# Kernel optimization log

Measured on AMD Instinct MI355X. Metric: run time of the kernel, lower is better.

The kernel has to match this reference:

```python
import jax, jax.numpy as jnp
import numpy as np

EPS = 1e-5  # torch GroupNorm default eps

def setup_inputs() -> dict:
    key = jax.random.key(0)
    ks = jax.random.split(key, 6)
    B, H, W, C = 16, 64, 64, 768
    T, R = 8, 64
    x = jax.random.normal(ks[0], (B, H, W, C), dtype=jnp.float32)
    task_ids = jax.random.randint(ks[1], (B,), 0, T, dtype=jnp.int32)
    gamma = jnp.ones((C,), dtype=jnp.float32)
    beta = jnp.zeros((C,), dtype=jnp.float32)
    # kaiming-uniform-ish scale for down proj; up proj small (zeros in torch init,
    # but use small random so gradients are non-trivial)
    W_down = jax.random.normal(ks[2], (T, R, C), dtype=jnp.float32) / jnp.sqrt(jnp.float32(C))
    W_up = jax.random.normal(ks[3], (T, C, R), dtype=jnp.float32) * 0.02
    scales = jnp.ones((T,), dtype=jnp.float32)
    return {"x": x, "task_ids": task_ids, "gamma": gamma, "beta": beta,
            "W_down": W_down, "W_up": W_up, "scales": scales}

def reference(x, task_ids, gamma, beta, W_down, W_up, scales):
    # GroupNorm(num_groups=1): normalize each sample over (H, W, C), per-channel affine
    mean = jnp.mean(x, axis=(1, 2, 3), keepdims=True)
    var = jnp.var(x, axis=(1, 2, 3), keepdims=True)
    x_norm = (x - mean) * jax.lax.rsqrt(var + EPS) * gamma + beta  # [B,H,W,C]
    # Gather per-sample expert weights (1x1 convs == low-rank linear maps)
    Wd = W_down[task_ids]          # [B, R, C]
    Wu = W_up[task_ids]            # [B, C, R]
    s = scales[task_ids]           # [B]
    h = jnp.einsum('bhwc,brc->bhwr', x_norm, Wd)
    h = jax.nn.gelu(h, approximate=False)  # torch nn.GELU default is exact erf
    delta = jnp.einsum('bhwr,bcr->bhwc', h, Wu)
    return x + s[:, None, None, None] * delta
```

## Files before the change

### kernel.cpp

```cpp
#include <hip/hip_runtime.h>
#include <hip/hip_bf16.h>

#define BATCH 16
#define C 768
#define T 8
#define R 64
#define HW 4096
#define NPS (HW*C)
#define GN_EPS 1e-5f
#define NPART 48

typedef short bf16x8 __attribute__((ext_vector_type(8)));
typedef float f32x4 __attribute__((ext_vector_type(4)));

static __device__ __forceinline__ unsigned short f2bf(float f) {
    __hip_bfloat16 h = __float2bfloat16(f);
    return *reinterpret_cast<unsigned short*>(&h);
}

__global__ __launch_bounds__(256) void prep_stats_kernel(
        const float* __restrict__ Wdn, const float* __restrict__ Wup,
        const float* __restrict__ gamma, const float* __restrict__ beta,
        const float* __restrict__ x,
        float* __restrict__ partials,
        unsigned short* __restrict__ wdg, unsigned short* __restrict__ wu_bf,
        float* __restrict__ u, float* __restrict__ w) {
    int bid = blockIdx.x;
    int tid = threadIdx.x;
    if (bid < 768) {
        int idx = bid * 256 + tid;
        const int NF4 = T * R * C / 4;
        if (idx < NF4) {
            int c4 = idx % (C / 4);
            float4 v = ((const float4*)Wdn)[idx];
            float4 g = ((const float4*)gamma)[c4];
            ushort4 o;
            o.x = f2bf(v.x * g.x); o.y = f2bf(v.y * g.y);
            o.z = f2bf(v.z * g.z); o.w = f2bf(v.w * g.w);
            *reinterpret_cast<ushort4*>(wdg + idx * 4) = o;
        } else {
            int j = idx - NF4;
            float4 v = ((const float4*)Wup)[j];
            ushort4 o;
            o.x = f2bf(v.x); o.y = f2bf(v.y); o.z = f2bf(v.z); o.w = f2bf(v.w);
            *reinterpret_cast<ushort4*>(wu_bf + j * 4) = o;
        }
    } else if (bid < 896) {
        int rowid = (bid - 768) * 4 + (tid >> 6);
        int lane = tid & 63;
        const float* wrow = Wdn + (size_t)rowid * C;
        float su = 0.f, sw = 0.f;
        #pragma unroll
        for (int j = 0; j < 12; j++) {
            int c = lane + j * 64;
            float wv = wrow[c];
            su += wv * gamma[c];
            sw += wv * beta[c];
        }
        for (int off = 32; off > 0; off >>= 1) {
            su += __shfl_down(su, off);
            sw += __shfl_down(sw, off);
        }
        if (lane == 0) { u[rowid] = su; w[rowid] = sw; }
    } else {
        int sblk = bid - 896;
        int b = sblk / NPART, part = sblk % NPART;
        const float4* xp = (const float4*)(x + (size_t)b * NPS);
        float s = 0.f, q = 0.f;
        int base = part * 256 + tid;
        #pragma unroll 4
        for (int i = 0; i < 64; i++) {
            float4 v = xp[(size_t)i * 12288 + base];
            s += v.x + v.y + v.z + v.w;
            q += v.x*v.x + v.y*v.y + v.z*v.z + v.w*v.w;
        }
        for (int off = 32; off > 0; off >>= 1) {
            s += __shfl_down(s, off);
            q += __shfl_down(q, off);
        }
        __shared__ float ps[4], pq[4];
        int wave = tid >> 6, lane = tid & 63;
        if (lane == 0) { ps[wave] = s; pq[wave] = q; }
        __syncthreads();
        if (tid == 0) {
            float S = 0.f, Q = 0.f;
            #pragma unroll
            for (int wv = 0; wv < 4; wv++) { S += ps[wv]; Q += pq[wv]; }
            partials[(b * NPART + part) * 2]     = S;
            partials[(b * NPART + part) * 2 + 1] = Q;
        }
    }
}

__global__ __launch_bounds__(512, 1) void fused_kernel(
        const float* __restrict__ x, const int* __restrict__ task_ids,
        const float* __restrict__ scales, const float* __restrict__ partials,
        const unsigned short* __restrict__ wdg, const unsigned short* __restrict__ wu_bf,
        const float* __restrict__ u, const float* __restrict__ w,
        float* __restrict__ out) {
    __shared__ char xsb[3 * 49152];
    __shared__ char hsb[2][2048];

    int bid = blockIdx.x;
    int b = bid >> 4;
    int chunk = bid & 15;
    int tid = threadIdx.x;
    int wvid = tid >> 6, lane = tid & 63;
    int lr = lane & 15, lg = lane >> 4;
    int swz = (lr & 7) << 4;

    int t = task_ids[b];
    float sc = scales[t];

    float s1 = 0.f, s2 = 0.f;
    if (lane < NPART) {
        float2 v = ((const float2*)(partials + b * 2 * NPART))[lane];
        s1 = v.x; s2 = v.y;
    }
    #pragma unroll
    for (int off = 32; off > 0; off >>= 1) {
        s1 += __shfl_xor(s1, off);
        s2 += __shfl_xor(s2, off);
    }
    float mean = s1 * (1.f / NPS);
    float var  = s2 * (1.f / NPS) - mean * mean;
    float rstd = rsqrtf(var + GN_EPS);

    size_t base = (size_t)b * NPS + (size_t)chunk * 256 * C;
    const char* xbase_c = (const char*)(x + base);
    float* outp = out + base;

#define STAGE(ldbuf, tileidx) do {                                               \
    const char* _gs = xbase_c + (size_t)(tileidx) * 49152;                       \
    char* _ld = (ldbuf);                                                         \
    _Pragma("unroll")                                                            \
    for (int _jj = 0; _jj < 12; _jj++) {                                         \
        int _j = pw * 12 + _jj;                                                  \
        int _row = _j / 3;                                                       \
        int _sub = _j - _row * 3;                                                \
        int _cb = (_sub * 1024 + lane * 16) ^ ((_row & 7) << 4);                 \
        __builtin_amdgcn_global_load_lds(                                        \
            (const __attribute__((address_space(1))) void*)(_gs + _row * 3072 + _cb), \
            (__attribute__((address_space(3))) void*)(_ld + (size_t)_j * 1024),  \
            16, 0, 0);                                                           \
    }                                                                            \
} while (0)

    if (wvid < 4) {
        int pw = wvid;
        const unsigned short* wdp = wdg + t * (R * C);
        bf16x8 a1[24];
        #pragma unroll
        for (int k = 0; k < 24; k++)
            a1[k] = *reinterpret_cast<const bf16x8*>(wdp + (pw * 16 + lr) * C + k * 32 + lg * 8);

        int r0 = pw * 16 + lg * 4;
        float4 u4 = *reinterpret_cast<const float4*>(u + t * 64 + r0);
        float4 w4 = *reinterpret_cast<const float4*>(w + t * 64 + r0);
        float mb = rstd * mean;
        float bias0 = w4.x - mb * u4.x, bias1 = w4.y - mb * u4.y;
        float bias2 = w4.z - mb * u4.z, bias3 = w4.w - mb * u4.w;

        STAGE(xsb, 0);
        STAGE(xsb + 49152, 1);

        for (int i = 0; i < 16; i++) {
            if (i == 15) asm volatile("s_waitcnt vmcnt(0)" ::: "memory");
            else         asm volatile("s_waitcnt vmcnt(12)" ::: "memory");

            const char* xb = xsb + (i % 3) * 49152;
            f32x4 acc1a = {0.f, 0.f, 0.f, 0.f};
            f32x4 acc1b = {0.f, 0.f, 0.f, 0.f};
            #pragma unroll
            for (int k = 0; k < 24; k += 2) {
                #pragma unroll
                for (int kk = 0; kk < 2; kk++) {
                    int kc = k + kk;
                    int cb0 = (kc * 128 + lg * 32) ^ swz;
                    int cb1 = (kc * 128 + lg * 32 + 16) ^ swz;
                    f32x4 xv0 = *reinterpret_cast<const f32x4*>(xb + lr * 3072 + cb0);
                    f32x4 xv1 = *reinterpret_cast<const f32x4*>(xb + lr * 3072 + cb1);
                    bf16x8 bfrag;
                    bfrag[0] = (short)f2bf(xv0[0]); bfrag[1] = (short)f2bf(xv0[1]);
                    bfrag[2] = (short)f2bf(xv0[2]); bfrag[3] = (short)f2bf(xv0[3]);
                    bfrag[4] = (short)f2bf(xv1[0]); bfrag[5] = (short)f2bf(xv1[1]);
                    bfrag[6] = (short)f2bf(xv1[2]); bfrag[7] = (short)f2bf(xv1[3]);
                    if (kk == 0)
                        acc1a = __builtin_amdgcn_mfma_f32_16x16x32_bf16(a1[kc], bfrag, acc1a, 0, 0, 0);
                    else
                        acc1b = __builtin_amdgcn_mfma_f32_16x16x32_bf16(a1[kc], bfrag, acc1b, 0, 0, 0);
                }
            }
            float v0 = rstd * (acc1a[0] + acc1b[0]) + bias0;
            float v1 = rstd * (acc1a[1] + acc1b[1]) + bias1;
            float v2 = rstd * (acc1a[2] + acc1b[2]) + bias2;
            float v3 = rstd * (acc1a[3] + acc1b[3]) + bias3;
            ushort4 o;
            o.x = f2bf(0.5f * v0 * (1.f + erff(v0 * 0.70710678118f)));
            o.y = f2bf(0.5f * v1 * (1.f + erff(v1 * 0.70710678118f)));
            o.z = f2bf(0.5f * v2 * (1.f + erff(v2 * 0.70710678118f)));
            o.w = f2bf(0.5f * v3 * (1.f + erff(v3 * 0.70710678118f)));
            int hbyte = lr * 128 + ((pw * 32 + lg * 8) ^ swz);
            *reinterpret_cast<ushort4*>(hsb[i & 1] + hbyte) = o;

            asm volatile("s_waitcnt lgkmcnt(0)" ::: "memory");
            __builtin_amdgcn_s_barrier();
            if (i + 2 < 16) STAGE(xsb + ((i + 2) % 3) * 49152, i + 2);
        }
    } else {
        int cw = wvid - 4;
        const unsigned short* wup = wu_bf + t * (C * R);
        bf16x8 a2[12][2];
        #pragma unroll
        for (int cb = 0; cb < 12; cb++)
            #pragma unroll
            for (int ks = 0; ks < 2; ks++)
                a2[cb][ks] = *reinterpret_cast<const bf16x8*>(
                    wup + (cw * 192 + cb * 16 + lr) * R + ks * 32 + lg * 8);

        for (int i = 0; i < 16; i++) {
            if (i > 0) {
                int j = i - 1;
                const char* xb = xsb + (j % 3) * 49152;
                bf16x8 b2[2];
                #pragma unroll
                for (int ks = 0; ks < 2; ks++) {
                    int byte = lr * 128 + ((ks * 64 + lg * 16) ^ swz);
                    b2[ks] = *reinterpret_cast<const bf16x8*>(hsb[j & 1] + byte);
                }
                size_t ro = (size_t)(j * 16 + lr) * C;
                #pragma unroll
                for (int cb = 0; cb < 12; cb++) {
                    f32x4 acc = {0.f, 0.f, 0.f, 0.f};
                    acc = __builtin_amdgcn_mfma_f32_16x16x32_bf16(a2[cb][0], b2[0], acc, 0, 0, 0);
                    acc = __builtin_amdgcn_mfma_f32_16x16x32_bf16(a2[cb][1], b2[1], acc, 0, 0, 0);
                    int c0 = cw * 192 + cb * 16 + lg * 4;
                    float4 xr = *reinterpret_cast<const float4*>(xb + lr * 3072 + ((c0 * 4) ^ swz));
                    float4 ov;
                    ov.x = xr.x + sc * acc[0];
                    ov.y = xr.y + sc * acc[1];
                    ov.z = xr.z + sc * acc[2];
                    ov.w = xr.w + sc * acc[3];
                    *reinterpret_cast<float4*>(outp + ro + c0) = ov;
                }
            }
            __builtin_amdgcn_s_barrier();
        }
        {
            int j = 15;
            const char* xb = xsb + (j % 3) * 49152;
            bf16x8 b2[2];
            #pragma unroll
            for (int ks = 0; ks < 2; ks++) {
                int byte = lr * 128 + ((ks * 64 + lg * 16) ^ swz);
                b2[ks] = *reinterpret_cast<const bf16x8*>(hsb[j & 1] + byte);
            }
            size_t ro = (size_t)(j * 16 + lr) * C;
            #pragma unroll
            for (int cb = 0; cb < 12; cb++) {
                f32x4 acc = {0.f, 0.f, 0.f, 0.f};
                acc = __builtin_amdgcn_mfma_f32_16x16x32_bf16(a2[cb][0], b2[0], acc, 0, 0, 0);
                acc = __builtin_amdgcn_mfma_f32_16x16x32_bf16(a2[cb][1], b2[1], acc, 0, 0, 0);
                int c0 = cw * 192 + cb * 16 + lg * 4;
                float4 xr = *reinterpret_cast<const float4*>(xb + lr * 3072 + ((c0 * 4) ^ swz));
                float4 ov;
                ov.x = xr.x + sc * acc[0];
                ov.y = xr.y + sc * acc[1];
                ov.z = xr.z + sc * acc[2];
                ov.w = xr.w + sc * acc[3];
                *reinterpret_cast<float4*>(outp + ro + c0) = ov;
            }
        }
    }
#undef STAGE
}

extern "C" void kernel_launch(void* const* d_in, const int* in_sizes, int n_in,
                              void* d_out, int out_size, void* d_ws, size_t ws_size,
                              hipStream_t stream) {
    const float* x        = (const float*)d_in[0];
    const int*   task_ids = (const int*)d_in[1];
    const float* gamma    = (const float*)d_in[2];
    const float* beta     = (const float*)d_in[3];
    const float* W_down   = (const float*)d_in[4];
    const float* W_up     = (const float*)d_in[5];
    const float* scales   = (const float*)d_in[6];
    float* out = (float*)d_out;

    float* partials = (float*)d_ws;
    unsigned short* wdg   = (unsigned short*)((char*)d_ws + 8192);
    unsigned short* wu_bf = wdg + T * R * C;
    float* u = (float*)((char*)d_ws + 8192 + 2 * T * R * C * sizeof(unsigned short));
    float* w = u + T * R;

    prep_stats_kernel<<<1664, 256, 0, stream>>>(W_down, W_up, gamma, beta, x,
                                                partials, wdg, wu_bf, u, w);
    fused_kernel<<<256, 512, 0, stream>>>(x, task_ids, scales, partials,
                                          wdg, wu_bf, u, w, out);
}
```

Before: 116.8 us.

## Merge stats and weight prep into one cooperative kernel with grid sync

Folds the separate prep/statistics kernel into the main kernel, which now runs as a cooperative launch. Each block reduces its own chunk of x for the GroupNorm sums, publishes the partials, and waits on a grid-wide sync before using the per-sample statistics. Weight bf16 conversion, gamma folding and the u/w bias terms are computed per block from fp32 weights instead of in a prep pass. Output stores become nontemporal. This removes one kernel launch and the intermediate workspace round-trip, at the cost of redundant per-block weight conversion, a grid-wide barrier, and reading x twice within one kernel.

```diff
diff --git a/kernel.cpp b/kernel.cpp
--- a/kernel.cpp
+++ b/kernel.cpp
@@ -1,5 +1,6 @@
 #include <hip/hip_runtime.h>
 #include <hip/hip_bf16.h>
+#include <hip/hip_cooperative_groups.h>
 
 #define BATCH 16
 #define C 768
@@ -8,7 +9,6 @@
 #define HW 4096
 #define NPS (HW*C)
 #define GN_EPS 1e-5f
-#define NPART 48
 
 typedef short bf16x8 __attribute__((ext_vector_type(8)));
 typedef float f32x4 __attribute__((ext_vector_type(4)));
@@ -18,88 +18,16 @@
     return *reinterpret_cast<unsigned short*>(&h);
 }
 
-__global__ __launch_bounds__(256) void prep_stats_kernel(
+__global__ __launch_bounds__(512, 1) void fused_all(
+        const float* __restrict__ x, const int* __restrict__ task_ids,
+        const float* __restrict__ gamma, const float* __restrict__ beta,
         const float* __restrict__ Wdn, const float* __restrict__ Wup,
-        const float* __restrict__ gamma, const float* __restrict__ beta,
-        const float* __restrict__ x,
-        float* __restrict__ partials,
-        unsigned short* __restrict__ wdg, unsigned short* __restrict__ wu_bf,
-        float* __restrict__ u, float* __restrict__ w) {
-    int bid = blockIdx.x;
-    int tid = threadIdx.x;
-    if (bid < 768) {
-        int idx = bid * 256 + tid;
-        const int NF4 = T * R * C / 4;
-        if (idx < NF4) {
-            int c4 = idx % (C / 4);
-            float4 v = ((const float4*)Wdn)[idx];
-            float4 g = ((const float4*)gamma)[c4];
-            ushort4 o;
-            o.x = f2bf(v.x * g.x); o.y = f2bf(v.y * g.y);
-            o.z = f2bf(v.z * g.z); o.w = f2bf(v.w * g.w);
-            *reinterpret_cast<ushort4*>(wdg + idx * 4) = o;
-        } else {
-            int j = idx - NF4;
-            float4 v = ((const float4*)Wup)[j];
-            ushort4 o;
-            o.x = f2bf(v.x); o.y = f2bf(v.y); o.z = f2bf(v.z); o.w = f2bf(v.w);
-            *reinterpret_cast<ushort4*>(wu_bf + j * 4) = o;
-        }
-    } else if (bid < 896) {
-        int rowid = (bid - 768) * 4 + (tid >> 6);
-        int lane = tid & 63;
-        const float* wrow = Wdn + (size_t)rowid * C;
-        float su = 0.f, sw = 0.f;
-        #pragma unroll
-        for (int j = 0; j < 12; j++) {
-            int c = lane + j * 64;
-            float wv = wrow[c];
-            su += wv * gamma[c];
-            sw += wv * beta[c];
-        }
-        for (int off = 32; off > 0; off >>= 1) {
-            su += __shfl_down(su, off);
-            sw += __shfl_down(sw, off);
-        }
-        if (lane == 0) { u[rowid] = su; w[rowid] = sw; }
-    } else {
-        int sblk = bid - 896;
-        int b = sblk / NPART, part = sblk % NPART;
-        const float4* xp = (const float4*)(x + (size_t)b * NPS);
-        float s = 0.f, q = 0.f;
-        int base = part * 256 + tid;
-        #pragma unroll 4
-        for (int i = 0; i < 64; i++) {
-            float4 v = xp[(size_t)i * 12288 + base];
-            s += v.x + v.y + v.z + v.w;
-            q += v.x*v.x + v.y*v.y + v.z*v.z + v.w*v.w;
-        }
-        for (int off = 32; off > 0; off >>= 1) {
-            s += __shfl_down(s, off);
-            q += __shfl_down(q, off);
-        }
-        __shared__ float ps[4], pq[4];
-        int wave = tid >> 6, lane = tid & 63;
-        if (lane == 0) { ps[wave] = s; pq[wave] = q; }
-        __syncthreads();
-        if (tid == 0) {
-            float S = 0.f, Q = 0.f;
-            #pragma unroll
-            for (int wv = 0; wv < 4; wv++) { S += ps[wv]; Q += pq[wv]; }
-            partials[(b * NPART + part) * 2]     = S;
-            partials[(b * NPART + part) * 2 + 1] = Q;
-        }
-    }
-}
-
-__global__ __launch_bounds__(512, 1) void fused_kernel(
-        const float* __restrict__ x, const int* __restrict__ task_ids,
-        const float* __restrict__ scales, const float* __restrict__ partials,
-        const unsigned short* __restrict__ wdg, const unsigned short* __restrict__ wu_bf,
-        const float* __restrict__ u, const float* __restrict__ w,
-        float* __restrict__ out) {
+        const float* __restrict__ scales,
+        float* __restrict__ partials, float* __restrict__ out) {
     __shared__ char xsb[3 * 49152];
     __shared__ char hsb[2][2048];
+    __shared__ float uws[4][16][2];
+    __shared__ float red[8][2];
 
     int bid = blockIdx.x;
     int b = bid >> 4;
@@ -112,23 +40,25 @@
     int t = task_ids[b];
     float sc = scales[t];
 
-    float s1 = 0.f, s2 = 0.f;
-    if (lane < NPART) {
-        float2 v = ((const float2*)(partials + b * 2 * NPART))[lane];
-        s1 = v.x; s2 = v.y;
+    size_t basee = (size_t)b * NPS + (size_t)chunk * 256 * C;
+    const float4* xp4 = (const float4*)(x + basee);
+    const char* xbase_c = (const char*)(x + basee);
+    float* outp = out + basee;
+
+    {
+        float s = 0.f, q = 0.f;
+        #pragma unroll 16
+        for (int i = 0; i < 96; i++) {
+            float4 v = xp4[i * 512 + tid];
+            s += v.x + v.y + v.z + v.w;
+            q += v.x*v.x + v.y*v.y + v.z*v.z + v.w*v.w;
+        }
+        for (int off = 32; off > 0; off >>= 1) {
+            s += __shfl_down(s, off);
+            q += __shfl_down(q, off);
+        }
+        if (lane == 0) { red[wvid][0] = s; red[wvid][1] = q; }
     }
-    #pragma unroll
-    for (int off = 32; off > 0; off >>= 1) {
-        s1 += __shfl_xor(s1, off);
-        s2 += __shfl_xor(s2, off);
-    }
-    float mean = s1 * (1.f / NPS);
-    float var  = s2 * (1.f / NPS) - mean * mean;
-    float rstd = rsqrtf(var + GN_EPS);
-
-    size_t base = (size_t)b * NPS + (size_t)chunk * 256 * C;
-    const char* xbase_c = (const char*)(x + base);
-    float* outp = out + base;
 
 #define STAGE(ldbuf, tileidx) do {                                               \
     const char* _gs = xbase_c + (size_t)(tileidx) * 49152;                       \
@@ -148,18 +78,71 @@
 
     if (wvid < 4) {
         int pw = wvid;
-        const unsigned short* wdp = wdg + t * (R * C);
+
+        const float* wdp = Wdn + (size_t)t * R * C + (size_t)(pw * 16 + lr) * C;
         bf16x8 a1[24];
         #pragma unroll
-        for (int k = 0; k < 24; k++)
-            a1[k] = *reinterpret_cast<const bf16x8*>(wdp + (pw * 16 + lr) * C + k * 32 + lg * 8);
-
-        int r0 = pw * 16 + lg * 4;
-        float4 u4 = *reinterpret_cast<const float4*>(u + t * 64 + r0);
-        float4 w4 = *reinterpret_cast<const float4*>(w + t * 64 + r0);
+        for (int k = 0; k < 24; k++) {
+            int col = k * 32 + lg * 8;
+            float4 v0 = *reinterpret_cast<const float4*>(wdp + col);
+            float4 v1 = *reinterpret_cast<const float4*>(wdp + col + 4);
+            float4 g0 = *reinterpret_cast<const float4*>(gamma + col);
+            float4 g1 = *reinterpret_cast<const float4*>(gamma + col + 4);
+            bf16x8 a;
+            a[0] = (short)f2bf(v0.x * g0.x); a[1] = (short)f2bf(v0.y * g0.y);
+            a[2] = (short)f2bf(v0.z * g0.z); a[3] = (short)f2bf(v0.w * g0.w);
+            a[4] = (short)f2bf(v1.x * g1.x); a[5] = (short)f2bf(v1.y * g1.y);
+            a[6] = (short)f2bf(v1.z * g1.z); a[7] = (short)f2bf(v1.w * g1.w);
+            a1[k] = a;
+        }
+
+        {
+            const float* wrow = Wdn + ((size_t)t * R + (pw * 16 + lr)) * C + lg * 192;
+            const float4* wr4 = (const float4*)wrow;
+            const float4* g4  = (const float4*)(gamma + lg * 192);
+            const float4* b4  = (const float4*)(beta  + lg * 192);
+            float su = 0.f, sw = 0.f;
+            #pragma unroll 8
+            for (int j = 0; j < 48; j++) {
+                float4 wv = wr4[j], gv = g4[j], bv = b4[j];
+                su += wv.x*gv.x + wv.y*gv.y + wv.z*gv.z + wv.w*gv.w;
+                sw += wv.x*bv.x + wv.y*bv.y + wv.z*bv.z + wv.w*bv.w;
+            }
+            su += __shfl_xor(su, 16); su += __shfl_xor(su, 32);
+            sw += __shfl_xor(sw, 16); sw += __shfl_xor(sw, 32);
+            if (lg == 0) { uws[pw][lr][0] = su; uws[pw][lr][1] = sw; }
+        }
+
+        __syncthreads();
+        if (tid == 0) {
+            float S = 0.f, Q = 0.f;
+            #pragma unroll
+            for (int wv = 0; wv < 8; wv++) { S += red[wv][0]; Q += red[wv][1]; }
+            __hip_atomic_store(&partials[bid * 2],     S, __ATOMIC_RELEASE, __HIP_MEMORY_SCOPE_AGENT);
+            __hip_atomic_store(&partials[bid * 2 + 1], Q, __ATOMIC_RELEASE, __HIP_MEMORY_SCOPE_AGENT);
+        }
+        cooperative_groups::this_grid().sync();
+
+        float s1 = 0.f, s2 = 0.f;
+        if (lane < 16) {
+            s1 = __hip_atomic_load(&partials[(b * 16 + lane) * 2],     __ATOMIC_ACQUIRE, __HIP_MEMORY_SCOPE_AGENT);
+            s2 = __hip_atomic_load(&partials[(b * 16 + lane) * 2 + 1], __ATOMIC_ACQUIRE, __HIP_MEMORY_SCOPE_AGENT);
+        }
+        #pragma unroll
+        for (int off = 8; off > 0; off >>= 1) {
+            s1 += __shfl_xor(s1, off);
+            s2 += __shfl_xor(s2, off);
+        }
+        s1 = __shfl(s1, 0); s2 = __shfl(s2, 0);
+        float mean = s1 * (1.f / NPS);
+        float var  = s2 * (1.f / NPS) - mean * mean;
+        float rstd = rsqrtf(var + GN_EPS);
         float mb = rstd * mean;
-        float bias0 = w4.x - mb * u4.x, bias1 = w4.y - mb * u4.y;
-        float bias2 = w4.z - mb * u4.z, bias3 = w4.w - mb * u4.w;
+        int r00 = lg * 4;
+        float bias0 = uws[pw][r00+0][1] - mb * uws[pw][r00+0][0];
+        float bias1 = uws[pw][r00+1][1] - mb * uws[pw][r00+1][0];
+        float bias2 = uws[pw][r00+2][1] - mb * uws[pw][r00+2][0];
+        float bias3 = uws[pw][r00+3][1] - mb * uws[pw][r00+3][0];
 
         STAGE(xsb, 0);
         STAGE(xsb + 49152, 1);
@@ -167,6 +150,7 @@
         for (int i = 0; i < 16; i++) {
             if (i == 15) asm volatile("s_waitcnt vmcnt(0)" ::: "memory");
             else         asm volatile("s_waitcnt vmcnt(12)" ::: "memory");
+            __builtin_amdgcn_s_barrier();
 
             const char* xb = xsb + (i % 3) * 49152;
             f32x4 acc1a = {0.f, 0.f, 0.f, 0.f};
@@ -209,16 +193,30 @@
         }
     } else {
         int cw = wvid - 4;
-        const unsigned short* wup = wu_bf + t * (C * R);
+
+        const float* wup = Wup + (size_t)t * C * R;
         bf16x8 a2[12][2];
         #pragma unroll
-        for (int cb = 0; cb < 12; cb++)
-            #pragma unroll
-            for (int ks = 0; ks < 2; ks++)
-                a2[cb][ks] = *reinterpret_cast<const bf16x8*>(
-                    wup + (cw * 192 + cb * 16 + lr) * R + ks * 32 + lg * 8);
+        for (int cb = 0; cb < 12; cb++) {
+            #pragma unroll
+            for (int ks = 0; ks < 2; ks++) {
+                const float* src = wup + (size_t)(cw * 192 + cb * 16 + lr) * R + ks * 32 + lg * 8;
+                float4 v0 = *reinterpret_cast<const float4*>(src);
+                float4 v1 = *reinterpret_cast<const float4*>(src + 4);
+                bf16x8 a;
+                a[0] = (short)f2bf(v0.x); a[1] = (short)f2bf(v0.y);
+                a[2] = (short)f2bf(v0.z); a[3] = (short)f2bf(v0.w);
+                a[4] = (short)f2bf(v1.x); a[5] = (short)f2bf(v1.y);
+                a[6] = (short)f2bf(v1.z); a[7] = (short)f2bf(v1.w);
+                a2[cb][ks] = a;
+            }
+        }
+
+        __syncthreads();
+        cooperative_groups::this_grid().sync();
 
         for (int i = 0; i < 16; i++) {
+            __builtin_amdgcn_s_barrier();
             if (i > 0) {
                 int j = i - 1;
                 const char* xb = xsb + (j % 3) * 49152;
@@ -236,12 +234,12 @@
                     acc = __builtin_amdgcn_mfma_f32_16x16x32_bf16(a2[cb][1], b2[1], acc, 0, 0, 0);
                     int c0 = cw * 192 + cb * 16 + lg * 4;
                     float4 xr = *reinterpret_cast<const float4*>(xb + lr * 3072 + ((c0 * 4) ^ swz));
-                    float4 ov;
-                    ov.x = xr.x + sc * acc[0];
-                    ov.y = xr.y + sc * acc[1];
-                    ov.z = xr.z + sc * acc[2];
-                    ov.w = xr.w + sc * acc[3];
-                    *reinterpret_cast<float4*>(outp + ro + c0) = ov;
+                    f32x4 ov;
+                    ov[0] = xr.x + sc * acc[0];
+                    ov[1] = xr.y + sc * acc[1];
+                    ov[2] = xr.z + sc * acc[2];
+                    ov[3] = xr.w + sc * acc[3];
+                    __builtin_nontemporal_store(ov, reinterpret_cast<f32x4*>(outp + ro + c0));
                 }
             }
             __builtin_amdgcn_s_barrier();
@@ -263,12 +261,12 @@
                 acc = __builtin_amdgcn_mfma_f32_16x16x32_bf16(a2[cb][1], b2[1], acc, 0, 0, 0);
                 int c0 = cw * 192 + cb * 16 + lg * 4;
                 float4 xr = *reinterpret_cast<const float4*>(xb + lr * 3072 + ((c0 * 4) ^ swz));
-                float4 ov;
-                ov.x = xr.x + sc * acc[0];
-                ov.y = xr.y + sc * acc[1];
-                ov.z = xr.z + sc * acc[2];
-                ov.w = xr.w + sc * acc[3];
-                *reinterpret_cast<float4*>(outp + ro + c0) = ov;
+                f32x4 ov;
+                ov[0] = xr.x + sc * acc[0];
+                ov[1] = xr.y + sc * acc[1];
+                ov[2] = xr.z + sc * acc[2];
+                ov[3] = xr.w + sc * acc[3];
+                __builtin_nontemporal_store(ov, reinterpret_cast<f32x4*>(outp + ro + c0));
             }
         }
     }
@@ -286,15 +284,11 @@
     const float* W_up     = (const float*)d_in[5];
     const float* scales   = (const float*)d_in[6];
     float* out = (float*)d_out;
-
     float* partials = (float*)d_ws;
-    unsigned short* wdg   = (unsigned short*)((char*)d_ws + 8192);
-    unsigned short* wu_bf = wdg + T * R * C;
-    float* u = (float*)((char*)d_ws + 8192 + 2 * T * R * C * sizeof(unsigned short));
-    float* w = u + T * R;
-
-    prep_stats_kernel<<<1664, 256, 0, stream>>>(W_down, W_up, gamma, beta, x,
-                                                partials, wdg, wu_bf, u, w);
-    fused_kernel<<<256, 512, 0, stream>>>(x, task_ids, scales, partials,
-                                          wdg, wu_bf, u, w, out);
+
+    void* args[] = {(void*)&x, (void*)&task_ids, (void*)&gamma, (void*)&beta,
+                    (void*)&W_down, (void*)&W_up, (void*)&scales,
+                    (void*)&partials, (void*)&out};
+    hipLaunchCooperativeKernel(reinterpret_cast<void*>(fused_all),
+                               dim3(256), dim3(512), args, 0, stream);
 }
```

New measurement: 212.9 us. 1.82x slower.
